# Optimization experiments

Hardware: AMD Instinct MI355X
Metric: run time of the kernel (lower is better)

The kernel has to match this reference:

```python
import jax, jax.numpy as jnp
import numpy as np

B, C, H, W = 4, 128, 64, 64
CQ = C // 8  # query/key channels = 16


def setup_inputs() -> dict:
    key = jax.random.key(0)
    ks = jax.random.split(key, 8)
    s = 0.05
    return {
        "x": jax.random.normal(ks[0], (B, C, H, W), jnp.float32),
        "wq": jax.random.normal(ks[1], (CQ, C), jnp.float32) * s,
        "bq": jax.random.normal(ks[2], (CQ,), jnp.float32) * s,
        "wk": jax.random.normal(ks[3], (CQ, C), jnp.float32) * s,
        "bk": jax.random.normal(ks[4], (CQ,), jnp.float32) * s,
        "wv": jax.random.normal(ks[5], (C, C), jnp.float32) * s,
        "bv": jax.random.normal(ks[6], (C,), jnp.float32) * s,
        # original inits gamma to 0; use small nonzero so attention path is exercised
        "gamma": jax.random.normal(ks[7], (1,), jnp.float32) * 0.1,
    }


def reference(x, wq, bq, wk, bk, wv, bv, gamma):
    b, c, h, w = x.shape
    n = h * w
    xf = x.reshape(b, c, n)  # [B, C, N]
    # 1x1 convs are per-position linear maps over channels
    q = jnp.einsum("qc,bcn->bnq", wq, xf) + bq            # [B, N, Cq]
    k = jnp.einsum("qc,bcn->bqn", wk, xf) + bk[:, None]   # [B, Cq, N]
    v = jnp.einsum("oc,bcn->bon", wv, xf) + bv[:, None]   # [B, C, N]
    # unscaled scores, softmax over keys (last dim), as in the original
    attn = jax.nn.softmax(jnp.einsum("bnq,bqm->bnm", q, k), axis=-1)  # [B, N, N]
    # out = value @ attention^T : out[b,c,n] = sum_m v[b,c,m] * attn[b,n,m]
    out = jnp.einsum("bom,bnm->bon", v, attn)             # [B, C, N]
    return gamma[0] * out.reshape(b, c, h, w) + x
```

## Files before the change

### kernel.cpp

```cpp
#include <hip/hip_runtime.h>
#include <hip/hip_bf16.h>

typedef float f32x4  __attribute__((ext_vector_type(4)));
typedef float f32x16 __attribute__((ext_vector_type(16)));
typedef short s16x8  __attribute__((ext_vector_type(8)));

#define NB 4
#define NC 128
#define NNPOS 4096
#define KSP 8
#define LOG2E 1.44269504088896f

__device__ __forceinline__ short bf16s(float x) {
    __hip_bfloat16 h = __float2bfloat16(x);
    return *reinterpret_cast<short*>(&h);
}
__device__ __forceinline__ int packbf2(float lo, float hi) {
    __hip_bfloat162 t = __float22bfloat162_rn(float2{lo, hi});
    return *reinterpret_cast<int*>(&t);
}
__device__ __forceinline__ float bf2f(unsigned short u) {
    unsigned int v = ((unsigned int)u) << 16;
    return *reinterpret_cast<float*>(&v);
}
__device__ __forceinline__ float exp2fast(float x) {
    return __builtin_amdgcn_exp2f(x);
}

__global__ __launch_bounds__(256) void qkv_kernel(
    const float* __restrict__ x,
    const float* __restrict__ wq, const float* __restrict__ bq,
    const float* __restrict__ wk, const float* __restrict__ bk,
    const float* __restrict__ wv, const float* __restrict__ bv,
    short* __restrict__ qb, short* __restrict__ kb, short* __restrict__ vt)
{
    const int n0  = blockIdx.x * 32;
    const int b   = blockIdx.y;
    const int tid = threadIdx.x;
    const int w = tid >> 6, lane = tid & 63, quad = lane >> 4, nn = lane & 15;

    __shared__ __align__(16) short xsT[32 * 136];

    #pragma unroll
    for (int p = 0; p < 4; ++p) {
        int idx = tid + p * 256;
        int cc = idx >> 3, n4 = (idx & 7) * 4;
        f32x4 xv = *(const f32x4*)&x[((size_t)(b * NC + cc)) * NNPOS + n0 + n4];
        #pragma unroll
        for (int j = 0; j < 4; ++j)
            xsT[(n4 + j) * 136 + cc] = bf16s(xv[j]);
    }

    s16x8 af[3][4];
    bool  live[3];
    f32x4 biasv[3];
    #pragma unroll
    for (int t = 0; t < 3; ++t) {
        int rid = 3 * w + t;
        int R   = rid * 16;
        const float* wsrc = nullptr; const float* bsrc = nullptr; int row0 = 0;
        float scale = 1.0f;
        if (rid < 8)        { wsrc = wv; bsrc = bv; row0 = R; }
        else if (rid == 8)  { wsrc = wq; bsrc = bq; row0 = 0; scale = LOG2E; }
        else if (rid == 10) { wsrc = wk; bsrc = bk; row0 = 0; }
        live[t] = (wsrc != nullptr);
        #pragma unroll
        for (int r = 0; r < 4; ++r)
            biasv[t][r] = live[t] ? scale * bsrc[row0 + quad * 4 + r] : 0.0f;
        if (live[t]) {
            #pragma unroll
            for (int ks = 0; ks < 4; ++ks) {
                const float* src = wsrc + (size_t)(row0 + nn) * NC + ks * 32 + quad * 8;
                f32x4 wa = *(const f32x4*)src;
                f32x4 wb = *(const f32x4*)(src + 4);
                s16x8 f;
                #pragma unroll
                for (int j = 0; j < 4; ++j) {
                    f[j]     = bf16s(scale * wa[j]);
                    f[j + 4] = bf16s(scale * wb[j]);
                }
                af[t][ks] = f;
            }
        }
    }
    __syncthreads();

    f32x4 acc[3][2];
    #pragma unroll
    for (int t = 0; t < 3; ++t)
        #pragma unroll
        for (int nt = 0; nt < 2; ++nt)
            acc[t][nt] = biasv[t];

    #pragma unroll
    for (int nt = 0; nt < 2; ++nt) {
        s16x8 bf[4];
        #pragma unroll
        for (int ks = 0; ks < 4; ++ks)
            bf[ks] = *(const s16x8*)&xsT[(nt * 16 + nn) * 136 + ks * 32 + quad * 8];
        #pragma unroll
        for (int t = 0; t < 3; ++t)
            if (live[t])
                #pragma unroll
                for (int ks = 0; ks < 4; ++ks)
                    acc[t][nt] = __builtin_amdgcn_mfma_f32_16x16x32_bf16(af[t][ks], bf[ks], acc[t][nt], 0, 0, 0);
    }

    const int slot = (nn & 3) | ((nn & 4) << 1) | ((nn & 8) >> 1);

    #pragma unroll
    for (int t = 0; t < 3; ++t) {
        if (!live[t]) continue;
        int R = (3 * w + t) * 16;
        #pragma unroll
        for (int nt = 0; nt < 2; ++nt) {
            int n = n0 + nt * 16 + nn;
            int kg = (n0 + nt * 16) >> 4;
            #pragma unroll
            for (int r = 0; r < 4; ++r) {
                short v = bf16s(acc[t][nt][r]);
                int row = R + quad * 4 + r;
                if (row < 128) {
                    int ct = row >> 5, c31r = row & 31;
                    vt[((((size_t)b * 256 + kg) * 4 + ct) * 32 + c31r) * 16 + slot] = v;
                } else if (row < 144)
                    qb[((size_t)(b * NNPOS) + n) * 16 + (row - 128)] = v;
                else
                    kb[((size_t)(b * NNPOS) + n) * 16 + (row - 160)] = v;
            }
        }
    }
}

__global__ __launch_bounds__(256, 2) void attn_kernel(
    const short* __restrict__ qb, const short* __restrict__ kb,
    const short* __restrict__ vt,
    unsigned short* __restrict__ Ow, float* __restrict__ lw)
{
    const int s   = blockIdx.x;
    const int b   = blockIdx.z;
    const int tid = threadIdx.x;
    const int w = tid >> 6, lane = tid & 63, h = lane >> 5, c31 = lane & 31;

    const int qt0 = (blockIdx.y * 4 + w) * 64;

    s16x8 bq0 = *(const s16x8*)(qb + ((size_t)(b * NNPOS) + qt0      + c31) * 16 + h * 8);
    s16x8 bq1 = *(const s16x8*)(qb + ((size_t)(b * NNPOS) + qt0 + 32 + c31) * 16 + h * 8);

    f32x16 acc[2][4];
    #pragma unroll
    for (int qt = 0; qt < 2; ++qt)
        #pragma unroll
        for (int ct = 0; ct < 4; ++ct)
            #pragma unroll
            for (int r = 0; r < 16; ++r) acc[qt][ct][r] = 0.0f;
    float lp[2] = {0.f, 0.f};

    const short* kbp = kb + (size_t)(b * NNPOS) * 16;
    const short* vbp = vt + (size_t)b * (256 * 4 * 512);
    const int mbase = s * (NNPOS / KSP);
    const int kgbase = mbase >> 4;

    for (int it = 0; it < (NNPOS / KSP) / 64; ++it) {
        const int m0 = mbase + it * 64;
        const int kg0 = kgbase + it * 4;

        s16x8 ak0 = *(const s16x8*)(kbp + (size_t)(m0      + c31) * 16 + h * 8);
        s16x8 ak1 = *(const s16x8*)(kbp + (size_t)(m0 + 32 + c31) * 16 + h * 8);

        s16x8 vb[2][4];
        #pragma unroll
        for (int p = 0; p < 2; ++p)
            #pragma unroll
            for (int ct = 0; ct < 4; ++ct)
                vb[p][ct] = *(const s16x8*)(vbp +
                    (((size_t)(kg0 + p) * 4 + ct) << 9) + (c31 << 4) + (h << 3));

        f32x16 z;
        #pragma unroll
        for (int r = 0; r < 16; ++r) z[r] = 0.0f;
        f32x16 sc[2][2];
        sc[0][0] = __builtin_amdgcn_mfma_f32_32x32x16_bf16(ak0, bq0, z, 0, 0, 0);
        sc[0][1] = __builtin_amdgcn_mfma_f32_32x32x16_bf16(ak1, bq0, z, 0, 0, 0);
        sc[1][0] = __builtin_amdgcn_mfma_f32_32x32x16_bf16(ak0, bq1, z, 0, 0, 0);
        sc[1][1] = __builtin_amdgcn_mfma_f32_32x32x16_bf16(ak1, bq1, z, 0, 0, 0);

        s16x8 pa[2][4];
        #pragma unroll
        for (int qt = 0; qt < 2; ++qt)
            #pragma unroll
            for (int p = 0; p < 4; ++p) {
                const f32x16& sv = sc[qt][p >> 1];
                const int off = (p & 1) * 8;
                union { int i[4]; s16x8 v; } u;
                #pragma unroll
                for (int j = 0; j < 4; ++j) {
                    float p0 = exp2fast(sv[off + 2 * j]);
                    float p1 = exp2fast(sv[off + 2 * j + 1]);
                    lp[qt] += p0 + p1;
                    u.i[j] = packbf2(p0, p1);
                }
                pa[qt][p] = u.v;
            }

        #pragma unroll
        for (int p = 0; p < 2; ++p)
            #pragma unroll
            for (int ct = 0; ct < 4; ++ct)
                #pragma unroll
                for (int qt = 0; qt < 2; ++qt)
                    acc[qt][ct] = __builtin_amdgcn_mfma_f32_32x32x16_bf16(
                        pa[qt][p], vb[p][ct], acc[qt][ct], 0, 0, 0);

        #pragma unroll
        for (int p = 0; p < 2; ++p)
            #pragma unroll
            for (int ct = 0; ct < 4; ++ct)
                vb[p][ct] = *(const s16x8*)(vbp +
                    (((size_t)(kg0 + 2 + p) * 4 + ct) << 9) + (c31 << 4) + (h << 3));
        #pragma unroll
        for (int p = 0; p < 2; ++p)
            #pragma unroll
            for (int ct = 0; ct < 4; ++ct)
                #pragma unroll
                for (int qt = 0; qt < 2; ++qt)
                    acc[qt][ct] = __builtin_amdgcn_mfma_f32_32x32x16_bf16(
                        pa[qt][2 + p], vb[p][ct], acc[qt][ct], 0, 0, 0);
    }

    #pragma unroll
    for (int qt = 0; qt < 2; ++qt) {
        lp[qt] += __shfl_xor(lp[qt], 32, 64);
        if (lane < 32)
            lw[((size_t)(b * KSP + s)) * NNPOS + qt0 + qt * 32 + c31] = lp[qt];
    }

    #pragma unroll
    for (int qt = 0; qt < 2; ++qt)
        #pragma unroll
        for (int ct = 0; ct < 4; ++ct)
            #pragma unroll
            for (int r = 0; r < 16; ++r) {
                int q = qt0 + qt * 32 + (r & 3) + 8 * (r >> 2) + 4 * h;
                Ow[(((size_t)(b * KSP + s)) * NNPOS + q) * NC + ct * 32 + c31] =
                    (unsigned short)bf16s(acc[qt][ct][r]);
            }
}

__global__ __launch_bounds__(256) void combine_kernel(
    const unsigned short* __restrict__ Ow, const float* __restrict__ lw,
    const float* __restrict__ x, const float* __restrict__ gamma,
    float* __restrict__ out)
{
    const int n0  = blockIdx.x * 64;
    const int b   = blockIdx.y;
    const int tid = threadIdx.x;

    __shared__ float ot[128 * 65 + 64];
    float* lsum = ot + 128 * 65;

    if (tid < 64) {
        float sl = 0.f;
        #pragma unroll
        for (int sI = 0; sI < KSP; ++sI)
            sl += lw[((size_t)(b * KSP + sI)) * NNPOS + n0 + tid];
        lsum[tid] = sl;
    }
    __syncthreads();

    #pragma unroll
    for (int p = 0; p < 8; ++p) {
        int e = tid + p * 256;
        int cq = e & 31, n = e >> 5;
        float a0 = 0.f, a1 = 0.f, a2 = 0.f, a3 = 0.f;
        #pragma unroll
        for (int sI = 0; sI < KSP; ++sI) {
            const unsigned short* src = Ow +
                (((size_t)(b * KSP + sI)) * NNPOS + n0 + n) * NC + cq * 4;
            ushort4 u = *(const ushort4*)src;
            a0 += bf2f(u.x); a1 += bf2f(u.y); a2 += bf2f(u.z); a3 += bf2f(u.w);
        }
        float inv = 1.0f / lsum[n];
        ot[(cq * 4) * 65 + n]     = a0 * inv;
        ot[(cq * 4 + 1) * 65 + n] = a1 * inv;
        ot[(cq * 4 + 2) * 65 + n] = a2 * inv;
        ot[(cq * 4 + 3) * 65 + n] = a3 * inv;
    }
    __syncthreads();

    const float g = gamma[0];
    #pragma unroll
    for (int p = 0; p < 32; ++p) {
        int e = tid + p * 256;
        int n = e & 63, c = e >> 6;
        size_t a = ((size_t)(b * NC + c)) * NNPOS + n0 + n;
        out[a] = g * ot[c * 65 + n] + x[a];
    }
}

extern "C" void kernel_launch(void* const* d_in, const int* in_sizes, int n_in,
                              void* d_out, int out_size, void* d_ws, size_t ws_size,
                              hipStream_t stream) {
    const float* x     = (const float*)d_in[0];
    const float* wq    = (const float*)d_in[1];
    const float* bq    = (const float*)d_in[2];
    const float* wk    = (const float*)d_in[3];
    const float* bk    = (const float*)d_in[4];
    const float* wv    = (const float*)d_in[5];
    const float* bv    = (const float*)d_in[6];
    const float* gamma = (const float*)d_in[7];
    float* out = (float*)d_out;

    short* qb = (short*)d_ws;
    short* kb = qb + (size_t)NB * NNPOS * 16;
    short* vt = kb + (size_t)NB * NNPOS * 16;
    unsigned short* Ow = (unsigned short*)(vt + (size_t)NB * NC * NNPOS);
    float* lw = (float*)(Ow + (size_t)NB * KSP * NNPOS * NC);

    qkv_kernel<<<dim3(128, NB), 256, 0, stream>>>(x, wq, bq, wk, bk, wv, bv, qb, kb, vt);
    attn_kernel<<<dim3(KSP, 16, NB), 256, 0, stream>>>(qb, kb, vt, Ow, lw);
    combine_kernel<<<dim3(NNPOS / 64, NB), 256, 0, stream>>>(Ow, lw, x, gamma, out);
}
```

Before: 115.2 us.

## Split attention channel halves across waves and double-buffer K/V register loads

Each wave now handles 64 queries but only half of the 128 value channels, and the grid doubles along the query axis. This halves the accumulator registers and should raise occupancy. In exchange, the QK^T scores and exp2 work are computed twice, once per channel half. K and V fragments are prefetched one iteration ahead into double-buffered registers, and the PV MFMAs are interleaved per probability fragment so the full score tile need not be held at once.

```diff
diff --git a/kernel.cpp b/kernel.cpp
--- a/kernel.cpp
+++ b/kernel.cpp
@@ -141,56 +141,70 @@
     const int b   = blockIdx.z;
     const int tid = threadIdx.x;
     const int w = tid >> 6, lane = tid & 63, h = lane >> 5, c31 = lane & 31;
-
-    const int qt0 = (blockIdx.y * 4 + w) * 64;
+    const int chalf = w & 1;
+    const int qt0 = blockIdx.y * 128 + (w >> 1) * 64;
 
     s16x8 bq0 = *(const s16x8*)(qb + ((size_t)(b * NNPOS) + qt0      + c31) * 16 + h * 8);
     s16x8 bq1 = *(const s16x8*)(qb + ((size_t)(b * NNPOS) + qt0 + 32 + c31) * 16 + h * 8);
 
-    f32x16 acc[2][4];
+    f32x16 acc[2][2];
     #pragma unroll
     for (int qt = 0; qt < 2; ++qt)
         #pragma unroll
-        for (int ct = 0; ct < 4; ++ct)
-            #pragma unroll
-            for (int r = 0; r < 16; ++r) acc[qt][ct][r] = 0.0f;
+        for (int ctl = 0; ctl < 2; ++ctl)
+            #pragma unroll
+            for (int r = 0; r < 16; ++r) acc[qt][ctl][r] = 0.0f;
     float lp[2] = {0.f, 0.f};
 
     const short* kbp = kb + (size_t)(b * NNPOS) * 16;
     const short* vbp = vt + (size_t)b * (256 * 4 * 512);
     const int mbase = s * (NNPOS / KSP);
     const int kgbase = mbase >> 4;
-
+    const int voff = (c31 << 4) + (h << 3);
+
+    s16x8 ak[2][2];
+    s16x8 vb[2][4][2];
+
+    #pragma unroll
+    for (int kt = 0; kt < 2; ++kt)
+        ak[0][kt] = *(const s16x8*)(kbp + (size_t)(mbase + kt * 32 + c31) * 16 + h * 8);
+    #pragma unroll
+    for (int p = 0; p < 4; ++p)
+        #pragma unroll
+        for (int ctl = 0; ctl < 2; ++ctl)
+            vb[0][p][ctl] = *(const s16x8*)(vbp +
+                (((size_t)(kgbase + p) * 4 + (chalf * 2 + ctl)) << 9) + voff);
+
+    #pragma unroll
     for (int it = 0; it < (NNPOS / KSP) / 64; ++it) {
-        const int m0 = mbase + it * 64;
-        const int kg0 = kgbase + it * 4;
-
-        s16x8 ak0 = *(const s16x8*)(kbp + (size_t)(m0      + c31) * 16 + h * 8);
-        s16x8 ak1 = *(const s16x8*)(kbp + (size_t)(m0 + 32 + c31) * 16 + h * 8);
-
-        s16x8 vb[2][4];
-        #pragma unroll
-        for (int p = 0; p < 2; ++p)
-            #pragma unroll
-            for (int ct = 0; ct < 4; ++ct)
-                vb[p][ct] = *(const s16x8*)(vbp +
-                    (((size_t)(kg0 + p) * 4 + ct) << 9) + (c31 << 4) + (h << 3));
+        const int cur = it & 1, nxt = cur ^ 1;
+
+        if (it < (NNPOS / KSP) / 64 - 1) {
+            const int m1 = mbase + (it + 1) * 64;
+            const int kg1 = kgbase + (it + 1) * 4;
+            #pragma unroll
+            for (int kt = 0; kt < 2; ++kt)
+                ak[nxt][kt] = *(const s16x8*)(kbp + (size_t)(m1 + kt * 32 + c31) * 16 + h * 8);
+            #pragma unroll
+            for (int p = 0; p < 4; ++p)
+                #pragma unroll
+                for (int ctl = 0; ctl < 2; ++ctl)
+                    vb[nxt][p][ctl] = *(const s16x8*)(vbp +
+                        (((size_t)(kg1 + p) * 4 + (chalf * 2 + ctl)) << 9) + voff);
+        }
 
         f32x16 z;
         #pragma unroll
         for (int r = 0; r < 16; ++r) z[r] = 0.0f;
-        f32x16 sc[2][2];
-        sc[0][0] = __builtin_amdgcn_mfma_f32_32x32x16_bf16(ak0, bq0, z, 0, 0, 0);
-        sc[0][1] = __builtin_amdgcn_mfma_f32_32x32x16_bf16(ak1, bq0, z, 0, 0, 0);
-        sc[1][0] = __builtin_amdgcn_mfma_f32_32x32x16_bf16(ak0, bq1, z, 0, 0, 0);
-        sc[1][1] = __builtin_amdgcn_mfma_f32_32x32x16_bf16(ak1, bq1, z, 0, 0, 0);
-
-        s16x8 pa[2][4];
-        #pragma unroll
-        for (int qt = 0; qt < 2; ++qt)
+
+        #pragma unroll
+        for (int qt = 0; qt < 2; ++qt) {
+            s16x8 bqt = qt ? bq1 : bq0;
+            f32x16 s0 = __builtin_amdgcn_mfma_f32_32x32x16_bf16(ak[cur][0], bqt, z, 0, 0, 0);
+            f32x16 s1 = __builtin_amdgcn_mfma_f32_32x32x16_bf16(ak[cur][1], bqt, z, 0, 0, 0);
             #pragma unroll
             for (int p = 0; p < 4; ++p) {
-                const f32x16& sv = sc[qt][p >> 1];
+                const f32x16& sv = (p < 2) ? s0 : s1;
                 const int off = (p & 1) * 8;
                 union { int i[4]; s16x8 v; } u;
                 #pragma unroll
@@ -200,51 +214,33 @@
                     lp[qt] += p0 + p1;
                     u.i[j] = packbf2(p0, p1);
                 }
-                pa[qt][p] = u.v;
+                #pragma unroll
+                for (int ctl = 0; ctl < 2; ++ctl)
+                    acc[qt][ctl] = __builtin_amdgcn_mfma_f32_32x32x16_bf16(
+                        u.v, vb[cur][p][ctl], acc[qt][ctl], 0, 0, 0);
             }
-
-        #pragma unroll
-        for (int p = 0; p < 2; ++p)
-            #pragma unroll
-            for (int ct = 0; ct < 4; ++ct)
-                #pragma unroll
-                for (int qt = 0; qt < 2; ++qt)
-                    acc[qt][ct] = __builtin_amdgcn_mfma_f32_32x32x16_bf16(
-                        pa[qt][p], vb[p][ct], acc[qt][ct], 0, 0, 0);
-
-        #pragma unroll
-        for (int p = 0; p < 2; ++p)
-            #pragma unroll
-            for (int ct = 0; ct < 4; ++ct)
-                vb[p][ct] = *(const s16x8*)(vbp +
-                    (((size_t)(kg0 + 2 + p) * 4 + ct) << 9) + (c31 << 4) + (h << 3));
-        #pragma unroll
-        for (int p = 0; p < 2; ++p)
-            #pragma unroll
-            for (int ct = 0; ct < 4; ++ct)
-                #pragma unroll
-                for (int qt = 0; qt < 2; ++qt)
-                    acc[qt][ct] = __builtin_amdgcn_mfma_f32_32x32x16_bf16(
-                        pa[qt][2 + p], vb[p][ct], acc[qt][ct], 0, 0, 0);
+        }
     }
 
     #pragma unroll
     for (int qt = 0; qt < 2; ++qt) {
         lp[qt] += __shfl_xor(lp[qt], 32, 64);
-        if (lane < 32)
+        if (chalf == 0 && lane < 32)
             lw[((size_t)(b * KSP + s)) * NNPOS + qt0 + qt * 32 + c31] = lp[qt];
     }
 
     #pragma unroll
     for (int qt = 0; qt < 2; ++qt)
         #pragma unroll
-        for (int ct = 0; ct < 4; ++ct)
+        for (int ctl = 0; ctl < 2; ++ctl) {
+            const int c = (chalf * 2 + ctl) * 32 + c31;
             #pragma unroll
             for (int r = 0; r < 16; ++r) {
                 int q = qt0 + qt * 32 + (r & 3) + 8 * (r >> 2) + 4 * h;
-                Ow[(((size_t)(b * KSP + s)) * NNPOS + q) * NC + ct * 32 + c31] =
-                    (unsigned short)bf16s(acc[qt][ct][r]);
+                Ow[(((size_t)(b * KSP + s)) * NNPOS + q) * NC + c] =
+                    (unsigned short)bf16s(acc[qt][ctl][r]);
             }
+        }
 }
 
 __global__ __launch_bounds__(256) void combine_kernel(
@@ -318,6 +314,6 @@
     float* lw = (float*)(Ow + (size_t)NB * KSP * NNPOS * NC);
 
     qkv_kernel<<<dim3(128, NB), 256, 0, stream>>>(x, wq, bq, wk, bk, wv, bv, qb, kb, vt);
-    attn_kernel<<<dim3(KSP, 16, NB), 256, 0, stream>>>(qb, kb, vt, Ow, lw);
+    attn_kernel<<<dim3(KSP, 32, NB), 256, 0, stream>>>(qb, kb, vt, Ow, lw);
     combine_kernel<<<dim3(NNPOS / 64, NB), 256, 0, stream>>>(Ow, lw, x, gamma, out);
 }
```

New measurement: 173.7 us. +50.8%, slower.
